# Optimization experiments

Hardware: AMD Instinct MI355X
Metric: run time of the kernel (lower is better)

Reference implementation:

```python
import jax, jax.numpy as jnp
import numpy as np

BINS = 5
POINTS = 2
EPS_DIV = 1e-6
GN_GROUPS = 32
GN_EPS = 1e-5


def bilinear_sum(img, ys, xs):
    """Sum of bilinear samples with zero padding outside the image.
    img: (B, C, H, W); ys, xs: (B, K, H, W) absolute sample coords.
    Returns (B, C, H, W) = sum over K of bilinear(img, ys_k, xs_k)."""
    B, C, H, W = img.shape
    K = ys.shape[1]
    y0 = jnp.floor(ys)
    x0 = jnp.floor(xs)
    imgf = img.reshape(B, C, H * W)
    acc = jnp.zeros((B, C, K, H, W), img.dtype)
    for dy, dx in ((0, 0), (0, 1), (1, 0), (1, 1)):
        yi = y0 + dy
        xi = x0 + dx
        w = (1.0 - jnp.abs(ys - yi)) * (1.0 - jnp.abs(xs - xi))
        valid = (yi >= 0) & (yi <= H - 1) & (xi >= 0) & (xi <= W - 1)
        yc = jnp.clip(yi, 0, H - 1).astype(jnp.int32)
        xc = jnp.clip(xi, 0, W - 1).astype(jnp.int32)
        idx = (yc * W + xc).reshape(B, 1, K * H * W)
        g = jnp.take_along_axis(imgf, idx, axis=2).reshape(B, C, K, H, W)
        acc = acc + (w * valid.astype(img.dtype))[:, None] * g
    return acc.sum(axis=2)


def setup_inputs():
    key = jax.random.key(0)
    ks = jax.random.split(key, 6)
    B, C, H, W = 2, 256, 100, 152
    P, K = POINTS, BINS
    x = jax.random.normal(ks[0], (B, C, H, W), jnp.float32)
    offsets = jax.random.normal(ks[1], (B, P * K * 2, H, W), jnp.float32) * 2.0
    ef_w = jax.random.normal(ks[2], (P * C, C), jnp.float32) * 0.02
    ef_b = jnp.zeros((P * C,), jnp.float32)
    hm1_w = jax.random.normal(ks[3], (P, C, C), jnp.float32) * 0.02
    hm1_b = jnp.zeros((P, C), jnp.float32)
    hm2_w = jax.random.normal(ks[4], (P, C), jnp.float32) * 0.02
    hm2_b = jnp.zeros((P,), jnp.float32)
    merge_w = jax.random.normal(ks[5], (C, P * C), jnp.float32) * 0.02
    merge_b = jnp.zeros((C,), jnp.float32)
    gn_g = jnp.ones((C,), jnp.float32)
    gn_b = jnp.zeros((C,), jnp.float32)
    return {"x": x, "offsets": offsets, "ef_w": ef_w, "ef_b": ef_b,
            "hm1_w": hm1_w, "hm1_b": hm1_b, "hm2_w": hm2_w, "hm2_b": hm2_b,
            "merge_w": merge_w, "merge_b": merge_b, "gn_g": gn_g, "gn_b": gn_b}


def reference(x, offsets, ef_w, ef_b, hm1_w, hm1_b, hm2_w, hm2_b, merge_w, merge_b, gn_g, gn_b):
    B, C, H, W = x.shape
    P, K = POINTS, BINS
    # expand_feat: 1x1 conv C -> P*C
    ef = jnp.einsum('bchw,dc->bdhw', x, ef_w) + ef_b[None, :, None, None]
    efp = ef.reshape(B, P, C, H, W)
    # heatmap: grouped 1x1 conv (per-point) -> ReLU -> grouped 1x1 conv -> exp
    h = jax.nn.relu(jnp.einsum('bpchw,pdc->bpdhw', efp, hm1_w) + hm1_b[None, :, :, None, None])
    heat = jnp.exp(jnp.einsum('bpdhw,pd->bphw', h, hm2_w) + hm2_b[None, :, None, None])  # (B,P,H,W)
    # offsets: (B, P, K, 2, H, W) with channel layout [y, x] per bin.
    # base_offset cancels the [1,bins] kernel grid, so the deform conv with
    # all-ones weights is simply: sum over bins of bilinear samples at
    # (h + off_y, w + off_x).
    off = offsets.reshape(B, P, K, 2, H, W)
    hg = jnp.arange(H, dtype=x.dtype)[None, None, None, :, None]
    wg = jnp.arange(W, dtype=x.dtype)[None, None, None, None, :]
    ys = hg + off[:, :, :, 0]  # (B,P,K,H,W)
    xs = wg + off[:, :, :, 1]
    outs = []
    for p in range(P):
        # sample feat*heat (C channels) and heat (1 channel) together
        img = jnp.concatenate([efp[:, p] * heat[:, p][:, None], heat[:, p][:, None]], axis=1)
        s = bilinear_sum(img, ys[:, p], xs[:, p])  # (B, C+1, H, W)
        outs.append(s[:, :C] / (s[:, C:] + EPS_DIV))
    outs = jnp.concatenate(outs, axis=1)  # (B, P*C, H, W)
    merged = jnp.einsum('bchw,dc->bdhw', outs, merge_w) + merge_b[None, :, None, None]
    # GroupNorm(32, C) + ReLU
    g = merged.reshape(B, GN_GROUPS, C // GN_GROUPS, H, W)
    mu = g.mean(axis=(2, 3, 4), keepdims=True)
    var = g.var(axis=(2, 3, 4), keepdims=True)
    gn = ((g - mu) / jnp.sqrt(var + GN_EPS)).reshape(B, C, H, W)
    gn = gn * gn_g[None, :, None, None] + gn_b[None, :, None, None]
    return jax.nn.relu(gn)
```

## Files before the change

kernel.cpp:

```cpp
#include <hip/hip_runtime.h>

#define BINS 5
#define PTS  2
constexpr int Bx = 2, Cc = 256, Hh = 100, Ww = 152;
constexpr int HW = Hh * Ww;
constexpr int NTILE = 475;
constexpr float EPS_DIV = 1e-6f;
constexpr float GN_EPS  = 1e-5f;

typedef __attribute__((ext_vector_type(8)))  _Float16 hfrag;
typedef __attribute__((ext_vector_type(2)))  _Float16 h2;
typedef __attribute__((ext_vector_type(16))) float    f32x16;

__device__ __forceinline__ ushort f2h(float f) {
    return __builtin_bit_cast(ushort, (_Float16)f);
}
__device__ __forceinline__ float hlo(unsigned u) {
    return (float)__builtin_bit_cast(_Float16, (ushort)(u & 0xffffu));
}
__device__ __forceinline__ float hhi(unsigned u) {
    return (float)__builtin_bit_cast(_Float16, (ushort)(u >> 16));
}

#define GLL16(g, l) __builtin_amdgcn_global_load_lds( \
    (const __attribute__((address_space(1))) unsigned*)(g), \
    (__attribute__((address_space(3))) unsigned*)(l), 16, 0, 0)

#define MFMA32(a, b, c) __builtin_amdgcn_mfma_f32_32x32x16_f16(a, b, c, 0, 0, 0)

__global__ __launch_bounds__(256)
void k_pre(const float* __restrict__ efw, const float* __restrict__ w1,
           const float* __restrict__ mw, ushort* __restrict__ wb,
           const float* __restrict__ x, ushort* __restrict__ xbt)
{
    __shared__ float tile[32][33];
    const int bid = blockIdx.x;
    const int t = threadIdx.x;
    if (bid < 192) {
        int gid = bid * 256 + t;
        int i = gid * 8;
        int arr = i >> 17, off = i & 131071;
        const float* src = arr == 0 ? efw : (arr == 1 ? w1 : mw);
        float4 v0 = *(const float4*)(src + off);
        float4 v1 = *(const float4*)(src + off + 4);
        int outaddr;
        if (arr == 0) {
            int m = off >> 8, k = off & 255;
            outaddr = (((k >> 4) * 16 + (m >> 5)) * 64 + (m & 31) + 32 * ((k >> 3) & 1)) * 8;
        } else if (arr == 1) {
            int p = off >> 16, r = off & 65535;
            int m = r >> 8, k = r & 255;
            outaddr = p * 65536 +
                      (((k >> 4) * 8 + (m >> 5)) * 64 + (m & 31) + 32 * ((k >> 3) & 1)) * 8;
        } else {
            int m = off >> 9, k = off & 511;
            outaddr = (((k >> 4) * 8 + (m >> 5)) * 64 + (m & 31) + 32 * ((k >> 3) & 1)) * 8;
        }
        ushort o[8] = { f2h(v0.x), f2h(v0.y), f2h(v0.z), f2h(v0.w),
                        f2h(v1.x), f2h(v1.y), f2h(v1.z), f2h(v1.w) };
        *(uint4*)(wb + arr * 131072 + outaddr) = *(uint4*)o;
    } else {
        int r = bid - 192;
        const int b = r / 3800; r -= b * 3800;
        const int c0 = (r / 475) * 32;
        const int hw0 = (r % 475) * 32;
        const float* xb = x + ((size_t)b * Cc + c0) * HW + hw0;
        const int tx = t & 31, ty = t >> 5;
        #pragma unroll
        for (int rr = 0; rr < 4; rr++) {
            int c = ty + rr * 8;
            tile[c][tx] = xb[(size_t)c * HW + tx];
        }
        __syncthreads();
        const int hwl = t >> 3, c4 = (t & 7) * 4;
        ushort4 o = { f2h(tile[c4 + 0][hwl]), f2h(tile[c4 + 1][hwl]),
                      f2h(tile[c4 + 2][hwl]), f2h(tile[c4 + 3][hwl]) };
        *(ushort4*)&xbt[((size_t)b * HW + hw0 + hwl) * Cc + c0 + c4] = o;
    }
}

__global__ __launch_bounds__(512, 2)
void k_ef(const ushort* __restrict__ xbt, const ushort* __restrict__ wbe,
          const float* __restrict__ efb, ushort* __restrict__ efp)
{
    __shared__ ushort B0[64 * 256];
    __shared__ ushort B1[64 * 256];
    const int t = threadIdx.x;
    const int wv = t >> 6, ln = t & 63;
    const int l31 = ln & 31, lh = ln >> 5;
    const int b = blockIdx.y;
    const int tt0 = blockIdx.x * 2;
    const ushort* xb = xbt + (size_t)b * HW * Cc;

    hfrag A[2][16];
    #pragma unroll
    for (int mf = 0; mf < 2; mf++)
        #pragma unroll
        for (int ks = 0; ks < 16; ks++)
            A[mf][ks] = *(const hfrag*)&wbe[((ks * 16 + (wv * 2 + mf)) * 64 + ln) * 8];
    __builtin_amdgcn_sched_barrier(0);

    auto stageB = [&](int tt, ushort* dst) {
        int tp0 = tt * 64;
        #pragma unroll
        for (int j = 0; j < 4; j++) {
            int unit = j * 512 + t;
            int prow = unit >> 5, c8 = unit & 31;
            int pq = tp0 + prow; if (pq > HW - 1) pq = HW - 1;
            const ushort* g = xb + (size_t)pq * Cc + ((c8 ^ (prow & 7)) << 3);
            ushort* l = dst + (j * 512 + wv * 64) * 8;
            GLL16(g, l);
        }
    };
    stageB(tt0, B0);
    stageB(tt0 + 1, B1);
    __builtin_amdgcn_sched_barrier(0);
    asm volatile("s_waitcnt vmcnt(4)" ::: "memory");
    __builtin_amdgcn_s_barrier();
    __builtin_amdgcn_sched_barrier(0);

    auto compute = [&](int tt, const ushort* Bs) {
        f32x16 acc[2][2];
        #pragma unroll
        for (int mf = 0; mf < 2; mf++)
            #pragma unroll
            for (int pf = 0; pf < 2; pf++)
                #pragma unroll
                for (int r = 0; r < 16; r++) acc[mf][pf][r] = 0.f;
        #pragma unroll
        for (int ks = 0; ks < 16; ks++) {
            int c = ks * 2 + lh;
            #pragma unroll
            for (int pf = 0; pf < 2; pf++) {
                hfrag bf = *(const hfrag*)&Bs[(pf * 32 + l31) * 256 + ((c ^ (l31 & 7)) << 3)];
                acc[0][pf] = MFMA32(A[0][ks], bf, acc[0][pf]);
                acc[1][pf] = MFMA32(A[1][ks], bf, acc[1][pf]);
            }
        }
        const int tp0 = tt * 64;
        #pragma unroll
        for (int mf = 0; mf < 2; mf++) {
            int m0 = wv * 2 + mf;
            const int p_ = m0 >> 3;
            ushort* outb = efp + (size_t)((b * PTS + p_) * HW) * Cc;
            int chb = (m0 * 32) & 255;
            #pragma unroll
            for (int q = 0; q < 4; q++) {
                float4 bv = *(const float4*)&efb[m0 * 32 + q * 8 + 4 * lh];
                #pragma unroll
                for (int pf = 0; pf < 2; pf++) {
                    int px = tp0 + pf * 32 + l31;
                    if (px < HW) {
                        int ch = chb + q * 8 + 4 * lh;
                        ushort4 o = { f2h(acc[mf][pf][q * 4 + 0] + bv.x),
                                      f2h(acc[mf][pf][q * 4 + 1] + bv.y),
                                      f2h(acc[mf][pf][q * 4 + 2] + bv.z),
                                      f2h(acc[mf][pf][q * 4 + 3] + bv.w) };
                        *(ushort4*)&outb[(size_t)px * Cc + ch] = o;
                    }
                }
            }
        }
    };
    compute(tt0, B0);
    asm volatile("s_waitcnt vmcnt(0)" ::: "memory");
    __builtin_amdgcn_s_barrier();
    __builtin_amdgcn_sched_barrier(0);
    compute(tt0 + 1, B1);
}

__global__ __launch_bounds__(512, 2)
void k_heat(const ushort* __restrict__ efp, const ushort* __restrict__ wb1,
            const float* __restrict__ b1, const float* __restrict__ w2,
            const float* __restrict__ b2, float* __restrict__ heat)
{
    __shared__ ushort B0[64 * 256];
    __shared__ ushort B1[64 * 256];
    __shared__ float red[8][64];
    const int t = threadIdx.x;
    const int wv = t >> 6, ln = t & 63;
    const int l31 = ln & 31, lh = ln >> 5;
    const int zz = blockIdx.y;
    const int b = zz >> 1, p = zz & 1;
    const int tt0 = blockIdx.x * 2;
    const ushort* eb = efp + (size_t)((b * PTS + p) * HW) * Cc;
    const float* b1p = b1 + p * 256;
    const float* w2p = w2 + p * 256;
    const float b2v = b2[p];

    hfrag A[16];
    #pragma unroll
    for (int ks = 0; ks < 16; ks++)
        A[ks] = *(const hfrag*)&wb1[p * 65536 + ((ks * 8 + wv) * 64 + ln) * 8];
    __builtin_amdgcn_sched_barrier(0);

    auto stageB = [&](int tt, ushort* dst) {
        int tp0 = tt * 64;
        #pragma unroll
        for (int j = 0; j < 4; j++) {
            int unit = j * 512 + t;
            int prow = unit >> 5, c8 = unit & 31;
            int pq = tp0 + prow; if (pq > HW - 1) pq = HW - 1;
            const ushort* g = eb + (size_t)pq * Cc + ((c8 ^ (prow & 7)) << 3);
            ushort* l = dst + (j * 512 + wv * 64) * 8;
            GLL16(g, l);
        }
    };
    stageB(tt0, B0);
    stageB(tt0 + 1, B1);
    __builtin_amdgcn_sched_barrier(0);
    asm volatile("s_waitcnt vmcnt(4)" ::: "memory");
    __builtin_amdgcn_s_barrier();
    __builtin_amdgcn_sched_barrier(0);

    auto compute = [&](int tt, const ushort* Bs) {
        f32x16 acc[2];
        #pragma unroll
        for (int pf = 0; pf < 2; pf++)
            #pragma unroll
            for (int r = 0; r < 16; r++) acc[pf][r] = 0.f;
        #pragma unroll
        for (int ks = 0; ks < 16; ks++) {
            int c = ks * 2 + lh;
            #pragma unroll
            for (int pf = 0; pf < 2; pf++) {
                hfrag bf = *(const hfrag*)&Bs[(pf * 32 + l31) * 256 + ((c ^ (l31 & 7)) << 3)];
                acc[pf] = MFMA32(A[ks], bf, acc[pf]);
            }
        }
        float s[2] = {0.f, 0.f};
        #pragma unroll
        for (int q = 0; q < 4; q++) {
            float4 b1v = *(const float4*)&b1p[wv * 32 + q * 8 + 4 * lh];
            float4 w2v = *(const float4*)&w2p[wv * 32 + q * 8 + 4 * lh];
            #pragma unroll
            for (int pf = 0; pf < 2; pf++) {
                float h0 = acc[pf][q * 4 + 0] + b1v.x;
                float h1 = acc[pf][q * 4 + 1] + b1v.y;
                float h2_ = acc[pf][q * 4 + 2] + b1v.z;
                float h3 = acc[pf][q * 4 + 3] + b1v.w;
                s[pf] += w2v.x * (h0 > 0.f ? h0 : 0.f);
                s[pf] += w2v.y * (h1 > 0.f ? h1 : 0.f);
                s[pf] += w2v.z * (h2_ > 0.f ? h2_ : 0.f);
                s[pf] += w2v.w * (h3 > 0.f ? h3 : 0.f);
            }
        }
        s[0] += __shfl_xor(s[0], 32);
        s[1] += __shfl_xor(s[1], 32);
        if (lh == 0) {
            red[wv][l31]      = s[0];
            red[wv][32 + l31] = s[1];
        }
        asm volatile("s_waitcnt lgkmcnt(0)" ::: "memory");
        __builtin_amdgcn_s_barrier();
        if (t < 64) {
            float v = red[0][t] + red[1][t] + red[2][t] + red[3][t] +
                      red[4][t] + red[5][t] + red[6][t] + red[7][t];
            int px = tt * 64 + t;
            if (px < HW) heat[(size_t)(b * PTS + p) * HW + px] = expf(v + b2v);
        }
    };
    compute(tt0, B0);
    asm volatile("s_waitcnt vmcnt(0)" ::: "memory");
    __builtin_amdgcn_s_barrier();
    __builtin_amdgcn_sched_barrier(0);
    compute(tt0 + 1, B1);
}

__global__ __launch_bounds__(512, 8)
void k_sm(const ushort* __restrict__ efp, const float* __restrict__ heat,
          const float* __restrict__ offs, const ushort* __restrict__ wbm,
          const float* __restrict__ mb, ushort* __restrict__ mgb,
          float* __restrict__ part2)
{
    __shared__ ushort Bs[32 * 512];
    __shared__ unsigned s_w[2][32][20];
    __shared__ ushort   s_o[2][32][20];
    const int t = threadIdx.x;
    const int wv = t >> 6, ln = t & 63;
    const int l31 = ln & 31, lh = ln >> 5;
    const int bid = blockIdx.x;
    const int xcd = bid & 7, ii = bid >> 3;
    const int b = xcd >> 2;
    const int tile = (xcd & 3) * 119 + ii;
    if (tile >= NTILE) return;
    const int m0 = tile * 32;

    if (t < 32 * BINS * PTS) {
        int p = t / 160, r = t - p * 160;
        int j = r / BINS, k = r - (r / BINS) * BINS;
        int hw = m0 + j;
        int hh = hw / Ww, ww = hw - hh * Ww;
        const float* heat_bp = heat + (size_t)(b * PTS + p) * HW;
        int chy = (p * BINS + k) * 2;
        float oy = offs[((size_t)b * (PTS * BINS * 2) + chy)     * HW + hw];
        float ox = offs[((size_t)b * (PTS * BINS * 2) + chy + 1) * HW + hw];
        float ysf = (float)hh + oy;
        float xsf = (float)ww + ox;
        float y0 = floorf(ysf), x0 = floorf(xsf);
        #pragma unroll
        for (int dy = 0; dy < 2; dy++)
            #pragma unroll
            for (int dx = 0; dx < 2; dx++) {
                float yi = y0 + dy, xi = x0 + dx;
                float wgt = (1.f - fabsf(ysf - yi)) * (1.f - fabsf(xsf - xi));
                bool valid = (yi >= 0.f) && (yi <= (float)(Hh - 1)) &&
                             (xi >= 0.f) && (xi <= (float)(Ww - 1));
                int yc = (int)yi; yc = yc < 0 ? 0 : (yc > Hh - 1 ? Hh - 1 : yc);
                int xc = (int)xi; xc = xc < 0 ? 0 : (xc > Ww - 1 ? Ww - 1 : xc);
                int idx = yc * Ww + xc;
                float wh = valid ? wgt * heat_bp[idx] : 0.f;
                int slot = k * 4 + dy * 2 + dx;
                s_w[p][j][slot] = __float_as_uint(wh);
                s_o[p][j][slot] = (ushort)idx;
            }
    }
    __syncthreads();
    if (t < 64) {
        int p = t >> 5, px = t & 31;
        float s = 0.f;
        #pragma unroll
        for (int u = 0; u < 20; u++) s += __uint_as_float(s_w[p][px][u]);
        float inv = 1.f / (s + EPS_DIV);
        #pragma unroll
        for (int u = 0; u < 20; u++) {
            float w = __uint_as_float(s_w[p][px][u]) * inv;
            unsigned hw16 = (unsigned)f2h(w);
            s_w[p][px][u] = hw16 | (hw16 << 16);
        }
    }
    __syncthreads();

    {
        const int p = wv >> 2;
        const int jb = (wv & 3) * 8;
        const int g = p * 32 + l31;
        const char* efbase = (const char*)(efp + (size_t)((b * PTS + p) * HW) * Cc)
                             + l31 * 16;
        #pragma unroll
        for (int i2 = 0; i2 < 8; i2 += 2) {
            const int j = jb + i2 + lh;
            h2 a0 = (h2){0, 0}, a1 = (h2){0, 0}, a2 = (h2){0, 0}, a3 = (h2){0, 0};
            #pragma unroll
            for (int u = 0; u < 20; u++) {
                unsigned wu = s_w[p][j][u];
                unsigned idx = s_o[p][j][u];
                uint4 v = *(const uint4*)(efbase + ((size_t)idx << 9));
                h2 wp = __builtin_bit_cast(h2, wu);
                a0 += wp * __builtin_bit_cast(h2, v.x);
                a1 += wp * __builtin_bit_cast(h2, v.y);
                a2 += wp * __builtin_bit_cast(h2, v.z);
                a3 += wp * __builtin_bit_cast(h2, v.w);
            }
            uint4 o = { __builtin_bit_cast(unsigned, a0), __builtin_bit_cast(unsigned, a1),
                        __builtin_bit_cast(unsigned, a2), __builtin_bit_cast(unsigned, a3) };
            *(uint4*)&Bs[j * 512 + ((g ^ j) << 3)] = o;
        }
    }
    __syncthreads();

    f32x16 acc;
    #pragma unroll
    for (int r = 0; r < 16; r++) acc[r] = 0.f;
    #pragma unroll 1
    for (int c4 = 0; c4 < 4; c4++) {
        hfrag A8[8];
        #pragma unroll
        for (int k8 = 0; k8 < 8; k8++)
            A8[k8] = *(const hfrag*)&wbm[(((c4 * 8 + k8) * 8 + wv) * 64 + ln) * 8];
        #pragma unroll
        for (int k8 = 0; k8 < 8; k8++) {
            int c = (c4 * 8 + k8) * 2 + lh;
            hfrag bf = *(const hfrag*)&Bs[l31 * 512 + ((c ^ l31) << 3)];
            acc = MFMA32(A8[k8], bf, acc);
        }
    }

    const int px = m0 + l31;
    float sg[4] = {0.f, 0.f, 0.f, 0.f};
    float qg[4] = {0.f, 0.f, 0.f, 0.f};
    #pragma unroll
    for (int q = 0; q < 4; q++) {
        float4 bv = *(const float4*)&mb[wv * 32 + q * 8 + 4 * lh];
        #pragma unroll
        for (int r = 0; r < 4; r++) {
            float bb = r == 0 ? bv.x : (r == 1 ? bv.y : (r == 2 ? bv.z : bv.w));
            float v = acc[q * 4 + r] + bb;
            int ch = wv * 32 + q * 8 + 4 * lh + r;
            mgb[((size_t)b * Cc + ch) * HW + px] = f2h(v);
            sg[q] += v; qg[q] += v * v;
        }
    }
    #pragma unroll
    for (int q = 0; q < 4; q++) {
        #pragma unroll
        for (int off = 1; off <= 32; off <<= 1) {
            sg[q] += __shfl_xor(sg[q], off);
            qg[q] += __shfl_xor(qg[q], off);
        }
    }
    if (ln == 0) {
        #pragma unroll
        for (int q = 0; q < 4; q++) {
            int g = wv * 4 + q;
            size_t idx = ((size_t)(b * 32 + g) * NTILE + tile) * 2;
            part2[idx + 0] = sg[q];
            part2[idx + 1] = qg[q];
        }
    }
}

__global__ __launch_bounds__(256)
void k_gnfinal(const float* __restrict__ part2, float* __restrict__ statf)
{
    const int bg = blockIdx.x;
    const int t = threadIdx.x;
    float s = 0.f, q = 0.f;
    for (int u = t; u < NTILE; u += 256) {
        s += part2[((size_t)bg * NTILE + u) * 2 + 0];
        q += part2[((size_t)bg * NTILE + u) * 2 + 1];
    }
    #pragma unroll
    for (int off = 1; off <= 32; off <<= 1) {
        s += __shfl_xor(s, off);
        q += __shfl_xor(q, off);
    }
    __shared__ float rs[4], rq[4];
    int wid = t >> 6;
    if ((t & 63) == 0) { rs[wid] = s; rq[wid] = q; }
    __syncthreads();
    if (t == 0) {
        float S = rs[0] + rs[1] + rs[2] + rs[3];
        float Q = rq[0] + rq[1] + rq[2] + rq[3];
        const float n = 8.f * HW;
        float mean = S / n;
        float var  = Q / n - mean * mean;
        statf[bg * 2 + 0] = mean;
        statf[bg * 2 + 1] = rsqrtf(var + GN_EPS);
    }
}

__global__ __launch_bounds__(256)
void k_gnapply(const ushort* __restrict__ mgb, const float* __restrict__ statf,
               const float* __restrict__ gg, const float* __restrict__ gb,
               float* __restrict__ out)
{
    const int i8 = blockIdx.x * 256 + threadIdx.x;
    const int i = i8 * 8;
    const int CHW = Cc * HW;
    const int b = i / CHW;
    const int r = i - b * CHW;
    const int c = r / HW;
    const int g = c >> 3;
    float mean = statf[(b * 32 + g) * 2 + 0];
    float istd = statf[(b * 32 + g) * 2 + 1];
    float sc = istd * gg[c];
    float sh = gb[c] - mean * sc;
    uint4 v = *(const uint4*)(mgb + i);
    float4 o0, o1;
    o0.x = fmaxf(hlo(v.x) * sc + sh, 0.f);
    o0.y = fmaxf(hhi(v.x) * sc + sh, 0.f);
    o0.z = fmaxf(hlo(v.y) * sc + sh, 0.f);
    o0.w = fmaxf(hhi(v.y) * sc + sh, 0.f);
    o1.x = fmaxf(hlo(v.z) * sc + sh, 0.f);
    o1.y = fmaxf(hhi(v.z) * sc + sh, 0.f);
    o1.z = fmaxf(hlo(v.w) * sc + sh, 0.f);
    o1.w = fmaxf(hhi(v.w) * sc + sh, 0.f);
    *(float4*)(out + i)     = o0;
    *(float4*)(out + i + 4) = o1;
}

extern "C" void kernel_launch(void* const* d_in, const int* in_sizes, int n_in,
                              void* d_out, int out_size, void* d_ws, size_t ws_size,
                              hipStream_t stream)
{
    const float* x    = (const float*)d_in[0];
    const float* offs = (const float*)d_in[1];
    const float* efw  = (const float*)d_in[2];
    const float* efb  = (const float*)d_in[3];
    const float* w1   = (const float*)d_in[4];
    const float* b1   = (const float*)d_in[5];
    const float* w2   = (const float*)d_in[6];
    const float* b2   = (const float*)d_in[7];
    const float* mw   = (const float*)d_in[8];
    const float* mb   = (const float*)d_in[9];
    const float* gg   = (const float*)d_in[10];
    const float* gb   = (const float*)d_in[11];
    float* out = (float*)d_out;

    ushort* wb    = (ushort*)d_ws;
    ushort* wbe   = wb;
    ushort* wb1   = wb + 131072;
    ushort* wbm   = wb + 262144;
    ushort* efp   = wb + 393216;
    ushort* xbt   = efp + (size_t)Bx * PTS * HW * Cc;
    ushort* mgb   = xbt + (size_t)Bx * HW * Cc;
    float*  heat  = (float*)(mgb + (size_t)Bx * Cc * HW);
    float*  part2 = heat + (size_t)Bx * PTS * HW;
    float*  statf = part2 + (size_t)64 * NTILE * 2;

    dim3 blk(256);
    k_pre    <<<dim3(7792),             blk, 0, stream>>>(efw, w1, mw, wb, x, xbt);
    k_ef     <<<dim3(119, Bx),    dim3(512), 0, stream>>>(xbt, wbe, efb, efp);
    k_heat   <<<dim3(119, 4),     dim3(512), 0, stream>>>(efp, wb1, b1, w2, b2, heat);
    k_sm     <<<dim3(952),        dim3(512), 0, stream>>>(efp, heat, offs, wbm, mb, mgb, part2);
    k_gnfinal<<<dim3(64),               blk, 0, stream>>>(part2, statf);
    k_gnapply<<<dim3(Bx * Cc * HW / 8 / 256), blk, 0, stream>>>(mgb, statf, gg, gb, out);
}
```

Baseline: 197.6 us.

## Fuse sampling, merge GEMM and GroupNorm into one cooperative kernel with grid syncs

Replaces the k_sm, k_gnfinal and k_gnapply launches with a single cooperative kernel. Merge-conv results stay in registers across two grid-wide syncs, which compute the GroupNorm statistics and then apply normalization and ReLU directly. This removes the fp16 intermediate write and re-read of the merged tensor and two kernel launches. In exchange it adds two grid barriers and requires all 952 blocks to be co-resident; if the cooperative launch fails, the code falls back to the old three-kernel path.

```diff
diff --git a/kernel.cpp b/kernel.cpp
--- a/kernel.cpp
+++ b/kernel.cpp
@@ -1,4 +1,6 @@
 #include <hip/hip_runtime.h>
+#include <hip/hip_cooperative_groups.h>
+namespace cg = cooperative_groups;
 
 #define BINS 5
 #define PTS  2
@@ -27,6 +29,7 @@
     (__attribute__((address_space(3))) unsigned*)(l), 16, 0, 0)
 
 #define MFMA32(a, b, c) __builtin_amdgcn_mfma_f32_32x32x16_f16(a, b, c, 0, 0, 0)
+#define SB0() __builtin_amdgcn_sched_barrier(0)
 
 __global__ __launch_bounds__(256)
 void k_pre(const float* __restrict__ efw, const float* __restrict__ w1,
@@ -98,7 +101,7 @@
         #pragma unroll
         for (int ks = 0; ks < 16; ks++)
             A[mf][ks] = *(const hfrag*)&wbe[((ks * 16 + (wv * 2 + mf)) * 64 + ln) * 8];
-    __builtin_amdgcn_sched_barrier(0);
+    SB0();
 
     auto stageB = [&](int tt, ushort* dst) {
         int tp0 = tt * 64;
@@ -114,10 +117,10 @@
     };
     stageB(tt0, B0);
     stageB(tt0 + 1, B1);
-    __builtin_amdgcn_sched_barrier(0);
+    SB0();
     asm volatile("s_waitcnt vmcnt(4)" ::: "memory");
     __builtin_amdgcn_s_barrier();
-    __builtin_amdgcn_sched_barrier(0);
+    SB0();
 
     auto compute = [&](int tt, const ushort* Bs) {
         f32x16 acc[2][2];
@@ -165,7 +168,7 @@
     compute(tt0, B0);
     asm volatile("s_waitcnt vmcnt(0)" ::: "memory");
     __builtin_amdgcn_s_barrier();
-    __builtin_amdgcn_sched_barrier(0);
+    SB0();
     compute(tt0 + 1, B1);
 }
 
@@ -192,7 +195,7 @@
     #pragma unroll
     for (int ks = 0; ks < 16; ks++)
         A[ks] = *(const hfrag*)&wb1[p * 65536 + ((ks * 8 + wv) * 64 + ln) * 8];
-    __builtin_amdgcn_sched_barrier(0);
+    SB0();
 
     auto stageB = [&](int tt, ushort* dst) {
         int tp0 = tt * 64;
@@ -208,10 +211,10 @@
     };
     stageB(tt0, B0);
     stageB(tt0 + 1, B1);
-    __builtin_amdgcn_sched_barrier(0);
+    SB0();
     asm volatile("s_waitcnt vmcnt(4)" ::: "memory");
     __builtin_amdgcn_s_barrier();
-    __builtin_amdgcn_sched_barrier(0);
+    SB0();
 
     auto compute = [&](int tt, const ushort* Bs) {
         f32x16 acc[2];
@@ -263,8 +266,200 @@
     compute(tt0, B0);
     asm volatile("s_waitcnt vmcnt(0)" ::: "memory");
     __builtin_amdgcn_s_barrier();
-    __builtin_amdgcn_sched_barrier(0);
+    SB0();
     compute(tt0 + 1, B1);
+}
+
+__global__ __launch_bounds__(512, 8)
+void k_smgn(const ushort* __restrict__ efp, const float* __restrict__ heat,
+            const float* __restrict__ offs, const ushort* __restrict__ wbm,
+            const float* __restrict__ mb, const float* __restrict__ gg,
+            const float* __restrict__ gb, float* __restrict__ part2,
+            float* __restrict__ statf, float* __restrict__ out)
+{
+    __shared__ ushort Bs[32 * 512];
+    __shared__ unsigned s_w[2][32][20];
+    __shared__ ushort   s_o[2][32][20];
+    const int t = threadIdx.x;
+    const int wv = t >> 6, ln = t & 63;
+    const int l31 = ln & 31, lh = ln >> 5;
+    const int bid = blockIdx.x;
+    const int xcd = bid & 7, ii = bid >> 3;
+    const int b = xcd >> 2;
+    const int tile = (xcd & 3) * 119 + ii;
+    const bool active = (tile < NTILE);
+    const int m0 = tile * 32;
+
+    f32x16 acc;
+    #pragma unroll
+    for (int r = 0; r < 16; r++) acc[r] = 0.f;
+
+    if (active) {
+        if (t < 32 * BINS * PTS) {
+            int p = t / 160, r = t - p * 160;
+            int j = r / BINS, k = r - (r / BINS) * BINS;
+            int hw = m0 + j;
+            int hh = hw / Ww, ww = hw - hh * Ww;
+            const float* heat_bp = heat + (size_t)(b * PTS + p) * HW;
+            int chy = (p * BINS + k) * 2;
+            float oy = offs[((size_t)b * (PTS * BINS * 2) + chy)     * HW + hw];
+            float ox = offs[((size_t)b * (PTS * BINS * 2) + chy + 1) * HW + hw];
+            float ysf = (float)hh + oy;
+            float xsf = (float)ww + ox;
+            float y0 = floorf(ysf), x0 = floorf(xsf);
+            #pragma unroll
+            for (int dy = 0; dy < 2; dy++)
+                #pragma unroll
+                for (int dx = 0; dx < 2; dx++) {
+                    float yi = y0 + dy, xi = x0 + dx;
+                    float wgt = (1.f - fabsf(ysf - yi)) * (1.f - fabsf(xsf - xi));
+                    bool valid = (yi >= 0.f) && (yi <= (float)(Hh - 1)) &&
+                                 (xi >= 0.f) && (xi <= (float)(Ww - 1));
+                    int yc = (int)yi; yc = yc < 0 ? 0 : (yc > Hh - 1 ? Hh - 1 : yc);
+                    int xc = (int)xi; xc = xc < 0 ? 0 : (xc > Ww - 1 ? Ww - 1 : xc);
+                    int idx = yc * Ww + xc;
+                    float wh = valid ? wgt * heat_bp[idx] : 0.f;
+                    int slot = k * 4 + dy * 2 + dx;
+                    s_w[p][j][slot] = __float_as_uint(wh);
+                    s_o[p][j][slot] = (ushort)idx;
+                }
+        }
+        __syncthreads();
+        if (t < 64) {
+            int p = t >> 5, px = t & 31;
+            float s = 0.f;
+            #pragma unroll
+            for (int u = 0; u < 20; u++) s += __uint_as_float(s_w[p][px][u]);
+            float inv = 1.f / (s + EPS_DIV);
+            #pragma unroll
+            for (int u = 0; u < 20; u++) {
+                float w = __uint_as_float(s_w[p][px][u]) * inv;
+                unsigned hw16 = (unsigned)f2h(w);
+                s_w[p][px][u] = hw16 | (hw16 << 16);
+            }
+        }
+        __syncthreads();
+
+        {
+            const int p = wv >> 2;
+            const int jb = (wv & 3) * 8;
+            const int g = p * 32 + l31;
+            const char* efbase = (const char*)(efp + (size_t)((b * PTS + p) * HW) * Cc)
+                                 + l31 * 16;
+            #pragma unroll
+            for (int i2 = 0; i2 < 8; i2 += 2) {
+                const int j = jb + i2 + lh;
+                h2 a0 = (h2){0, 0}, a1 = (h2){0, 0}, a2 = (h2){0, 0}, a3 = (h2){0, 0};
+                #pragma unroll
+                for (int u = 0; u < 20; u++) {
+                    unsigned wu = s_w[p][j][u];
+                    unsigned idx = s_o[p][j][u];
+                    uint4 v = *(const uint4*)(efbase + ((size_t)idx << 9));
+                    h2 wp = __builtin_bit_cast(h2, wu);
+                    a0 += wp * __builtin_bit_cast(h2, v.x);
+                    a1 += wp * __builtin_bit_cast(h2, v.y);
+                    a2 += wp * __builtin_bit_cast(h2, v.z);
+                    a3 += wp * __builtin_bit_cast(h2, v.w);
+                }
+                uint4 o = { __builtin_bit_cast(unsigned, a0), __builtin_bit_cast(unsigned, a1),
+                            __builtin_bit_cast(unsigned, a2), __builtin_bit_cast(unsigned, a3) };
+                *(uint4*)&Bs[j * 512 + ((g ^ j) << 3)] = o;
+            }
+        }
+        __syncthreads();
+
+        #pragma unroll 1
+        for (int c4 = 0; c4 < 4; c4++) {
+            hfrag A8[8];
+            #pragma unroll
+            for (int k8 = 0; k8 < 8; k8++)
+                A8[k8] = *(const hfrag*)&wbm[(((c4 * 8 + k8) * 8 + wv) * 64 + ln) * 8];
+            #pragma unroll
+            for (int k8 = 0; k8 < 8; k8++) {
+                int c = (c4 * 8 + k8) * 2 + lh;
+                hfrag bf = *(const hfrag*)&Bs[l31 * 512 + ((c ^ l31) << 3)];
+                acc = MFMA32(A8[k8], bf, acc);
+            }
+        }
+        float sg[4] = {0.f, 0.f, 0.f, 0.f};
+        float qg[4] = {0.f, 0.f, 0.f, 0.f};
+        #pragma unroll
+        for (int q = 0; q < 4; q++) {
+            float4 bv = *(const float4*)&mb[wv * 32 + q * 8 + 4 * lh];
+            #pragma unroll
+            for (int r = 0; r < 4; r++) {
+                float bb = r == 0 ? bv.x : (r == 1 ? bv.y : (r == 2 ? bv.z : bv.w));
+                acc[q * 4 + r] += bb;
+                float v = acc[q * 4 + r];
+                sg[q] += v; qg[q] += v * v;
+            }
+        }
+        #pragma unroll
+        for (int q = 0; q < 4; q++) {
+            #pragma unroll
+            for (int off = 1; off <= 32; off <<= 1) {
+                sg[q] += __shfl_xor(sg[q], off);
+                qg[q] += __shfl_xor(qg[q], off);
+            }
+        }
+        if (ln == 0) {
+            #pragma unroll
+            for (int q = 0; q < 4; q++) {
+                int g = wv * 4 + q;
+                size_t idx = ((size_t)(b * 32 + g) * NTILE + tile) * 2;
+                part2[idx + 0] = sg[q];
+                part2[idx + 1] = qg[q];
+            }
+        }
+    }
+
+    cg::this_grid().sync();
+
+    if (bid < 64) {
+        float s = 0.f, q = 0.f;
+        for (int u = t; u < NTILE; u += 512) {
+            s += part2[((size_t)bid * NTILE + u) * 2 + 0];
+            q += part2[((size_t)bid * NTILE + u) * 2 + 1];
+        }
+        #pragma unroll
+        for (int off = 1; off <= 32; off <<= 1) {
+            s += __shfl_xor(s, off);
+            q += __shfl_xor(q, off);
+        }
+        float* red = (float*)Bs;
+        if (ln == 0) { red[wv * 2] = s; red[wv * 2 + 1] = q; }
+        __syncthreads();
+        if (t == 0) {
+            float S = 0.f, Q = 0.f;
+            #pragma unroll
+            for (int w = 0; w < 8; w++) { S += red[w * 2]; Q += red[w * 2 + 1]; }
+            const float n = 8.f * HW;
+            float mean = S / n;
+            float var  = Q / n - mean * mean;
+            statf[bid * 2 + 0] = mean;
+            statf[bid * 2 + 1] = rsqrtf(var + GN_EPS);
+        }
+    }
+
+    cg::this_grid().sync();
+
+    if (active) {
+        const int px = m0 + l31;
+        #pragma unroll
+        for (int q = 0; q < 4; q++) {
+            int g = wv * 4 + q;
+            float mean = statf[(b * 32 + g) * 2 + 0];
+            float istd = statf[(b * 32 + g) * 2 + 1];
+            #pragma unroll
+            for (int r = 0; r < 4; r++) {
+                int ch = wv * 32 + q * 8 + 4 * lh + r;
+                float sc = istd * gg[ch];
+                float sh = gb[ch] - mean * sc;
+                out[((size_t)b * Cc + ch) * HW + px] =
+                    fmaxf(acc[q * 4 + r] * sc + sh, 0.f);
+            }
+        }
+    }
 }
 
 __global__ __launch_bounds__(512, 8)
@@ -330,7 +525,6 @@
         }
     }
     __syncthreads();
-
     {
         const int p = wv >> 2;
         const int jb = (wv & 3) * 8;
@@ -375,7 +569,6 @@
             acc = MFMA32(A8[k8], bf, acc);
         }
     }
-
     const int px = m0 + l31;
     float sg[4] = {0.f, 0.f, 0.f, 0.f};
     float qg[4] = {0.f, 0.f, 0.f, 0.f};
@@ -503,7 +696,17 @@
     k_pre    <<<dim3(7792),             blk, 0, stream>>>(efw, w1, mw, wb, x, xbt);
     k_ef     <<<dim3(119, Bx),    dim3(512), 0, stream>>>(xbt, wbe, efb, efp);
     k_heat   <<<dim3(119, 4),     dim3(512), 0, stream>>>(efp, wb1, b1, w2, b2, heat);
-    k_sm     <<<dim3(952),        dim3(512), 0, stream>>>(efp, heat, offs, wbm, mb, mgb, part2);
-    k_gnfinal<<<dim3(64),               blk, 0, stream>>>(part2, statf);
-    k_gnapply<<<dim3(Bx * Cc * HW / 8 / 256), blk, 0, stream>>>(mgb, statf, gg, gb, out);
-}
+
+    const ushort* efp_c = efp;
+    const float*  heat_c = heat;
+    void* args[] = { (void*)&efp_c, (void*)&heat_c, (void*)&offs, (void*)&wbm,
+                     (void*)&mb, (void*)&gg, (void*)&gb, (void*)&part2,
+                     (void*)&statf, (void*)&out };
+    hipError_t e = hipLaunchCooperativeKernel((const void*)k_smgn, dim3(952),
+                                              dim3(512), args, 0, stream);
+    if (e != hipSuccess) {
+        k_sm     <<<dim3(952),     dim3(512), 0, stream>>>(efp, heat, offs, wbm, mb, mgb, part2);
+        k_gnfinal<<<dim3(64),            blk, 0, stream>>>(part2, statf);
+        k_gnapply<<<dim3(Bx * Cc * HW / 8 / 256), blk, 0, stream>>>(mgb, statf, gg, gb, out);
+    }
+}
```

Measured after the change: 458.0 us. +131.8%, slower.
